# Optimization experiments

Hardware: AMD Instinct MI355X
Metric: run time of the kernel (lower is better)

The kernel has to match this reference:

```python
import jax, jax.numpy as jnp
import numpy as np

NUM_HEADS = 16
DIM_HIDDEN = 1024
DIM_ATTN = DIM_HIDDEN // NUM_HEADS  # 64
SCALE = DIM_ATTN ** (-0.5)
TOP_K = 32


def setup_inputs() -> dict:
    rng = jax.random.key(0)
    k1, k2, k3, k4, k5 = jax.random.split(rng, 5)
    b, sq, sk, d = 2, 2048, 2048, DIM_HIDDEN
    lim = 1.0 / np.sqrt(d)  # nn.Linear default init range
    return {
        "query": jax.random.normal(k1, (b, sq, d), jnp.float32),
        "key": jax.random.normal(k2, (b, sk, d), jnp.float32),
        "value": jax.random.normal(k3, (b, sk, d), jnp.float32),
        "Wq": jax.random.uniform(k4, (d, d), jnp.float32, -lim, lim),
        "Wk": jax.random.uniform(k5, (d, d), jnp.float32, -lim, lim),
    }


def _split_heads(x, b, s):
    # (b, s, D) -> (b, H, s, d_head)
    return x.reshape(b, s, NUM_HEADS, DIM_ATTN).transpose(0, 2, 1, 3)


def reference(query, key, value, Wq, Wk):
    b, sq, d = query.shape
    sk = key.shape[1]
    # nn.Linear: y = x @ W^T  (bias=False); V and out are Identity
    q = _split_heads(query @ Wq.T, b, sq)
    k = _split_heads(key @ Wk.T, b, sk)
    v = _split_heads(value, b, sk)
    # dense scores (b, H, sq, sk)
    scores = jnp.einsum('bhqa,bhka->bhqk', q, k) * SCALE
    # top-k sparsified softmax: keep entries >= k-th largest score per row
    top_vals = jax.lax.top_k(scores, TOP_K)[0]
    cutoff = top_vals[..., -1:]  # (b, H, sq, 1)
    masked = jnp.where(scores >= cutoff, scores, -jnp.inf)
    w = jax.nn.softmax(masked, axis=-1)
    e = jnp.einsum('bhqk,bhka->bhqa', w, v)
    return e.transpose(0, 2, 1, 3).reshape(b, sq, d)
```

## Files before the change

### kernel.cpp

```cpp
#include <hip/hip_runtime.h>
#include <cstdint>
#include <cstddef>

#define BB 2
#define HH 16
#define SS 2048
#define DD 1024
#define DA 64
#define TOPK 32
#define ROWS 4

__global__ __launch_bounds__(256, 4) void proj_kernel(const float* __restrict__ X0,
                                                      const float* __restrict__ W0,
                                                      float* __restrict__ O0,
                                                      const float* __restrict__ X1,
                                                      const float* __restrict__ W1,
                                                      float* __restrict__ O1) {
  const float* __restrict__ X = blockIdx.z ? X1 : X0;
  const float* __restrict__ W = blockIdx.z ? W1 : W0;
  float* __restrict__ O       = blockIdx.z ? O1 : O0;

  __shared__ float Ast[16][64];
  __shared__ float Bst[16][64];
  const int tid = threadIdx.x;
  const int tx = tid & 15, ty = tid >> 4;
  const int m0 = blockIdx.y * 64, n0 = blockIdx.x * 64;

  float res[4][4], acc[4][4];
#pragma unroll
  for (int i = 0; i < 4; ++i)
#pragma unroll
    for (int j = 0; j < 4; ++j) { res[i][j] = 0.f; acc[i][j] = 0.f; }

  const int srow = tid >> 2, skg = tid & 3;
  for (int k0 = 0; k0 < 1024; k0 += 16) {
    if (k0 == 384 || k0 == 768) {
#pragma unroll
      for (int i = 0; i < 4; ++i)
#pragma unroll
        for (int j = 0; j < 4; ++j) { res[i][j] = __fadd_rn(res[i][j], acc[i][j]); acc[i][j] = 0.f; }
    }
    {
      const float4 va = *(const float4*)(X + (size_t)(m0 + srow) * 1024 + k0 + skg * 4);
      Ast[skg * 4 + 0][srow] = va.x; Ast[skg * 4 + 1][srow] = va.y;
      Ast[skg * 4 + 2][srow] = va.z; Ast[skg * 4 + 3][srow] = va.w;
      const float4 vb = *(const float4*)(W + (size_t)(n0 + srow) * 1024 + k0 + skg * 4);
      Bst[skg * 4 + 0][srow] = vb.x; Bst[skg * 4 + 1][srow] = vb.y;
      Bst[skg * 4 + 2][srow] = vb.z; Bst[skg * 4 + 3][srow] = vb.w;
    }
    __syncthreads();
#pragma unroll
    for (int k = 0; k < 16; ++k) {
      float av[4], bv[4];
#pragma unroll
      for (int i = 0; i < 4; ++i) av[i] = Ast[k][ty * 4 + i];
#pragma unroll
      for (int j = 0; j < 4; ++j) bv[j] = Bst[k][tx * 4 + j];
#pragma unroll
      for (int i = 0; i < 4; ++i)
#pragma unroll
        for (int j = 0; j < 4; ++j) acc[i][j] = fmaf(av[i], bv[j], acc[i][j]);
    }
    __syncthreads();
  }

#pragma unroll
  for (int i = 0; i < 4; ++i) {
    const int m = m0 + ty * 4 + i;
    const int b = m >> 11, s = m & 2047;
#pragma unroll
    for (int j = 0; j < 4; ++j) {
      const int n = n0 + tx * 4 + j;
      const int h = n >> 6, da = n & 63;
      const float v = __fadd_rn(res[i][j], acc[i][j]);
      if (blockIdx.z) {
        O[(((size_t)((b * 16 + h) * 16 + (da >> 2)) * 2048 + s) << 2) + (da & 3)] = v;
      } else {
        O[(((size_t)(b * 16 + h) * 2048 + s) * 64 + da)] = v;
      }
    }
  }
}

__global__ __launch_bounds__(256) void attn_kernel(const float* __restrict__ Qp,
                                                   const float* __restrict__ Kp,
                                                   const float* __restrict__ V,
                                                   float* __restrict__ out) {
  __shared__ float Srow[ROWS * 2048];

  const int tid = threadIdx.x;
  const int w = tid >> 6, l = tid & 63;
  const int nwg = BB * HH * (SS / ROWS);
  const int bidx = (int)blockIdx.x;
  const int swz = (bidx & 7) * (nwg >> 3) + (bidx >> 3);
  const int bh = swz >> 9;
  const int rb = swz & 511;
  const int b = bh >> 4, h = bh & 15;
  const int r0 = rb * ROWS;

  const float* Ktb = Kp + (size_t)bh * (16 * 2048 * 4);

#pragma unroll 1
  for (int c = 0; c < 8; ++c) {
    const int key = tid + c * 256;

    float acc[ROWS][4];
#pragma unroll
    for (int r = 0; r < ROWS; ++r)
#pragma unroll
      for (int j = 0; j < 4; ++j) acc[r][j] = 0.f;

#pragma unroll
    for (int g = 0; g < 4; ++g) {
      float4 kt[4];
#pragma unroll
      for (int i = 0; i < 4; ++i)
        kt[i] = *(const float4*)(Ktb + (((size_t)(g * 4 + i) * 2048 + key) << 2));
#pragma unroll
      for (int r = 0; r < ROWS; ++r) {
        const float4* qp4 = (const float4*)(Qp + ((size_t)bh * SS + r0 + r) * DA);
        float4 q4[4];
#pragma unroll
        for (int i = 0; i < 4; ++i) q4[i] = qp4[g * 4 + i];
#pragma unroll
        for (int blk = 3; blk >= 0; --blk) {
          acc[r][0] = __fadd_rn(acc[r][0], __fmul_rn(q4[blk].x, kt[blk].x));
          acc[r][1] = __fadd_rn(acc[r][1], __fmul_rn(q4[blk].y, kt[blk].y));
          acc[r][2] = __fadd_rn(acc[r][2], __fmul_rn(q4[blk].z, kt[blk].z));
          acc[r][3] = __fadd_rn(acc[r][3], __fmul_rn(q4[blk].w, kt[blk].w));
        }
      }
    }
#pragma unroll
    for (int r = 0; r < ROWS; ++r) {
      const float s = __fadd_rn(__fadd_rn(acc[r][0], acc[r][1]),
                                __fadd_rn(acc[r][2], acc[r][3]));
      Srow[r * 2048 + key] = s * 0.125f;
    }
  }
  __syncthreads();

  const float* Vh = V + (size_t)b * SS * DD + h * DA;
  float* outh = out + ((size_t)(b * SS + r0 + w)) * DD + h * DA;

  {
    const int r = w;
    float sv[32];
#pragma unroll
    for (int i = 0; i < 32; ++i) sv[i] = Srow[r * 2048 + 64 * i + l];
    float* wl = &Srow[r * 2048];
    float* kl = &Srow[r * 2048 + 64];

    float mx = sv[0], mn = sv[0];
#pragma unroll
    for (int i = 1; i < 32; ++i) { mx = fmaxf(mx, sv[i]); mn = fminf(mn, sv[i]); }
#pragma unroll
    for (int off = 32; off >= 1; off >>= 1) {
      mx = fmaxf(mx, __shfl_xor(mx, off));
      mn = fminf(mn, __shfl_xor(mn, off));
    }

    float lo = mn, hi = mx + 1.0f;
    float cutoff = mn;
    for (int it = 0; ; ++it) {
      const float mid = 0.5f * (lo + hi);
      if (it >= 64 || !(mid > lo && mid < hi)) { cutoff = lo; break; }
      int c = 0;
#pragma unroll
      for (int i = 0; i < 32; ++i)
        c += (int)__popcll(__ballot(sv[i] >= mid));
      if (c == TOPK) {
        float cm = 3.0e38f;
#pragma unroll
        for (int i = 0; i < 32; ++i) if (sv[i] >= mid) cm = fminf(cm, sv[i]);
#pragma unroll
        for (int off = 32; off >= 1; off >>= 1) cm = fminf(cm, __shfl_xor(cm, off));
        cutoff = cm;
        break;
      }
      if (c > TOPK) lo = mid; else hi = mid;
    }

    float wv[32];
    float dpart = 0.f;
    int ckept = 0;
#pragma unroll
    for (int i = 0; i < 32; ++i) {
      const bool keep = (sv[i] >= cutoff);
      ckept += (int)__popcll(__ballot(keep));
      const float e = keep ? __expf(sv[i] - mx) : 0.f;
      wv[i] = e;
      dpart += e;
    }
    float denom = dpart;
#pragma unroll
    for (int off = 32; off >= 1; off >>= 1) denom += __shfl_xor(denom, off);
    const float inv_denom = 1.0f / denom;

    float e = 0.f;
    if (ckept <= 64) {
      int base = 0;
#pragma unroll
      for (int i = 0; i < 32; ++i) {
        const unsigned long long mball = __ballot(wv[i] > 0.f);
        if (wv[i] > 0.f) {
          const int pos = base + (int)__popcll(mball & ((1ull << l) - 1ull));
          wl[pos] = wv[i];
          kl[pos] = __int_as_float(64 * i + l);
        }
        base += (int)__popcll(mball);
      }
      asm volatile("s_waitcnt lgkmcnt(0)" ::: "memory");
      int i = 0;
      for (; i + 8 <= ckept; i += 8) {
        float ww[8]; int kk[8];
#pragma unroll
        for (int u = 0; u < 8; ++u) { ww[u] = wl[i + u]; kk[u] = __float_as_int(kl[i + u]); }
        float vv[8];
#pragma unroll
        for (int u = 0; u < 8; ++u) vv[u] = Vh[(size_t)kk[u] * DD + l];
#pragma unroll
        for (int u = 0; u < 8; ++u) e = fmaf(ww[u], vv[u], e);
      }
      for (; i < ckept; ++i) {
        const float ww = wl[i];
        const int kk = __float_as_int(kl[i]);
        e = fmaf(ww, Vh[(size_t)kk * DD + l], e);
      }
    } else {
#pragma unroll
      for (int i = 0; i < 32; ++i) Srow[r * 2048 + 64 * i + l] = wv[i];
      asm volatile("s_waitcnt lgkmcnt(0)" ::: "memory");
      for (int k = 0; k < 2048; ++k) {
        const float ww = Srow[r * 2048 + k];
        if (ww > 0.f) e = fmaf(ww, Vh[(size_t)k * DD + l], e);
      }
    }
    outh[l] = e * inv_denom;
  }
}

extern "C" void kernel_launch(void* const* d_in, const int* in_sizes, int n_in,
                              void* d_out, int out_size, void* d_ws, size_t ws_size,
                              hipStream_t stream) {
  const float* query = (const float*)d_in[0];
  const float* key   = (const float*)d_in[1];
  const float* value = (const float*)d_in[2];
  const float* Wq    = (const float*)d_in[3];
  const float* Wk    = (const float*)d_in[4];
  float* out = (float*)d_out;

  float* Qp = (float*)d_ws;
  float* Kp = Qp + (size_t)BB * HH * SS * DA;

  proj_kernel<<<dim3(16, 64, 2), 256, 0, stream>>>(query, Wq, Qp, key, Wk, Kp);
  attn_kernel<<<dim3(BB * HH * (SS / ROWS)), 256, 0, stream>>>(Qp, Kp, value, out);
}
```

Measured before the change: 882.7 us.

## Double-buffer projection GEMM tiles with register prefetch and vectorized LDS stores

The projection kernel now keeps two LDS buffers. While the current tile is being computed, it prefetches the next K-tile of X and W into registers, which removes one barrier per iteration. Global loads change from float4 row reads to scalar strided reads so that each thread can write one float4 transposed into LDS. LDS reads in the inner loop also become float4. The goal is to overlap global latency with FMA work, at the cost of less coalesced global loads (16 consecutive floats per row group) and more LDS.

```diff
diff --git a/kernel.cpp b/kernel.cpp
--- a/kernel.cpp
+++ b/kernel.cpp
@@ -20,19 +20,36 @@
   const float* __restrict__ W = blockIdx.z ? W1 : W0;
   float* __restrict__ O       = blockIdx.z ? O1 : O0;
 
-  __shared__ float Ast[16][64];
-  __shared__ float Bst[16][64];
+  __shared__ float Ast[2][16][64];
+  __shared__ float Bst[2][16][64];
   const int tid = threadIdx.x;
   const int tx = tid & 15, ty = tid >> 4;
   const int m0 = blockIdx.y * 64, n0 = blockIdx.x * 64;
 
+  const int sk = tid & 15;
+  const int smg = tid >> 4;
+
   float res[4][4], acc[4][4];
 #pragma unroll
   for (int i = 0; i < 4; ++i)
 #pragma unroll
     for (int j = 0; j < 4; ++j) { res[i][j] = 0.f; acc[i][j] = 0.f; }
 
-  const int srow = tid >> 2, skg = tid & 3;
+  {
+    float xa[4], xb[4];
+#pragma unroll
+    for (int j = 0; j < 4; ++j) {
+      xa[j] = X[(size_t)(m0 + smg * 4 + j) * 1024 + sk];
+      xb[j] = W[(size_t)(n0 + smg * 4 + j) * 1024 + sk];
+    }
+    float4 va; va.x = xa[0]; va.y = xa[1]; va.z = xa[2]; va.w = xa[3];
+    float4 vb; vb.x = xb[0]; vb.y = xb[1]; vb.z = xb[2]; vb.w = xb[3];
+    *(float4*)&Ast[0][sk][smg * 4] = va;
+    *(float4*)&Bst[0][sk][smg * 4] = vb;
+  }
+  __syncthreads();
+
+  int cur = 0;
   for (int k0 = 0; k0 < 1024; k0 += 16) {
     if (k0 == 384 || k0 == 768) {
 #pragma unroll
@@ -40,28 +57,37 @@
 #pragma unroll
         for (int j = 0; j < 4; ++j) { res[i][j] = __fadd_rn(res[i][j], acc[i][j]); acc[i][j] = 0.f; }
     }
-    {
-      const float4 va = *(const float4*)(X + (size_t)(m0 + srow) * 1024 + k0 + skg * 4);
-      Ast[skg * 4 + 0][srow] = va.x; Ast[skg * 4 + 1][srow] = va.y;
-      Ast[skg * 4 + 2][srow] = va.z; Ast[skg * 4 + 3][srow] = va.w;
-      const float4 vb = *(const float4*)(W + (size_t)(n0 + srow) * 1024 + k0 + skg * 4);
-      Bst[skg * 4 + 0][srow] = vb.x; Bst[skg * 4 + 1][srow] = vb.y;
-      Bst[skg * 4 + 2][srow] = vb.z; Bst[skg * 4 + 3][srow] = vb.w;
+
+    const bool more = (k0 + 16) < 1024;
+    float ya[4], yb[4];
+    if (more) {
+#pragma unroll
+      for (int j = 0; j < 4; ++j) {
+        ya[j] = X[(size_t)(m0 + smg * 4 + j) * 1024 + (k0 + 16) + sk];
+        yb[j] = W[(size_t)(n0 + smg * 4 + j) * 1024 + (k0 + 16) + sk];
+      }
+    }
+
+#pragma unroll
+    for (int k = 0; k < 16; ++k) {
+      const float4 av4 = *(const float4*)&Ast[cur][k][ty * 4];
+      const float4 bv4 = *(const float4*)&Bst[cur][k][tx * 4];
+      const float av[4] = {av4.x, av4.y, av4.z, av4.w};
+      const float bv[4] = {bv4.x, bv4.y, bv4.z, bv4.w};
+#pragma unroll
+      for (int i = 0; i < 4; ++i)
+#pragma unroll
+        for (int j = 0; j < 4; ++j) acc[i][j] = fmaf(av[i], bv[j], acc[i][j]);
+    }
+
+    if (more) {
+      float4 va; va.x = ya[0]; va.y = ya[1]; va.z = ya[2]; va.w = ya[3];
+      float4 vb; vb.x = yb[0]; vb.y = yb[1]; vb.z = yb[2]; vb.w = yb[3];
+      *(float4*)&Ast[cur ^ 1][sk][smg * 4] = va;
+      *(float4*)&Bst[cur ^ 1][sk][smg * 4] = vb;
     }
     __syncthreads();
-#pragma unroll
-    for (int k = 0; k < 16; ++k) {
-      float av[4], bv[4];
-#pragma unroll
-      for (int i = 0; i < 4; ++i) av[i] = Ast[k][ty * 4 + i];
-#pragma unroll
-      for (int j = 0; j < 4; ++j) bv[j] = Bst[k][tx * 4 + j];
-#pragma unroll
-      for (int i = 0; i < 4; ++i)
-#pragma unroll
-        for (int j = 0; j < 4; ++j) acc[i][j] = fmaf(av[i], bv[j], acc[i][j]);
-    }
-    __syncthreads();
+    cur ^= 1;
   }
 
 #pragma unroll
```

New measurement: 1.997 ms. 2.26x slower.
